# Kernel optimization log

Measured on AMD Instinct MI355X. Metric: run time of the kernel, lower is better.

The kernel has to match this reference:

```python
import jax, jax.numpy as jnp
import numpy as np

QMAX = 127.0   # 8-bit symmetric quantization
BN_EPS = 1e-5
MID = 576      # in_channels * 6 expansion


def act_fake_quant(x):
    """Per-tensor symmetric 8-bit fake-quant of activations (HAWQ QuantAct).
    Returns dequantized value and the scaling factor. STE for gradients."""
    s = jax.lax.stop_gradient(jnp.max(jnp.abs(x)) / QMAX + 1e-8)
    q = jnp.clip(jnp.round(x / s), -QMAX, QMAX) * s
    return x + jax.lax.stop_gradient(q - x), s


def fold_bn(w, gamma, beta, mean, var):
    """Fold BN into conv weights/bias (QuantBnConv2d.set_param math)."""
    f = gamma / jnp.sqrt(var + BN_EPS)
    return w * f[:, None, None, None], beta - mean * f


def weight_fake_quant(w):
    """Per-output-channel symmetric 8-bit fake-quant of folded weights."""
    s = jax.lax.stop_gradient(jnp.max(jnp.abs(w), axis=(1, 2, 3)) / QMAX + 1e-8)
    sb = s[:, None, None, None]
    q = jnp.clip(jnp.round(w / sb), -QMAX, QMAX) * sb
    return w + jax.lax.stop_gradient(q - w), s


def qbn_conv(x, w, gamma, beta, mean, var, stride, groups, pad):
    """BN-folded, weight-quantized conv (QuantBnConv2d forward)."""
    wf, bf = fold_bn(w, gamma, beta, mean, var)
    wq, ws = weight_fake_quant(wf)
    y = jax.lax.conv_general_dilated(
        x, wq, window_strides=(stride, stride), padding=pad,
        dimension_numbers=('NCHW', 'OIHW', 'NCHW'), feature_group_count=groups)
    return y + bf[None, :, None, None], ws


def setup_inputs() -> dict:
    key = jax.random.key(0)
    ks = jax.random.split(key, 16)
    C_in, C_out = 96, 96
    d = {'x': jax.random.normal(ks[0], (64, C_in, 28, 28), jnp.float32)}
    def bn(k, c):
        k1, k2, k3, k4 = jax.random.split(k, 4)
        return (1.0 + 0.1 * jax.random.normal(k1, (c,), jnp.float32),   # gamma
                0.1 * jax.random.normal(k2, (c,), jnp.float32),          # beta
                0.1 * jax.random.normal(k3, (c,), jnp.float32),          # running mean
                0.5 + jax.random.uniform(k4, (c,), jnp.float32))         # running var
    # conv1: 1x1 expansion 96 -> 576
    d['w1'] = 0.1 * jax.random.normal(ks[1], (MID, C_in, 1, 1), jnp.float32)
    d['g1'], d['b1'], d['m1'], d['v1'] = bn(ks[2], MID)
    # conv2: 3x3 depthwise, groups=576
    d['w2'] = 0.1 * jax.random.normal(ks[3], (MID, 1, 3, 3), jnp.float32)
    d['g2'], d['b2'], d['m2'], d['v2'] = bn(ks[4], MID)
    # conv3: 1x1 projection 576 -> 96
    d['w3'] = 0.1 * jax.random.normal(ks[5], (C_out, MID, 1, 1), jnp.float32)
    d['g3'], d['b3'], d['m3'], d['v3'] = bn(ks[6], C_out)
    return d


def reference(x, w1, g1, b1, m1, v1, w2, g2, b2, m2, v2, w3, g3, b3, m3, v3):
    identity = x
    # quant_act on input
    y, act_sf = act_fake_quant(x)
    # conv1 (1x1 expansion) + ReLU6 + quant_act1
    y, _ = qbn_conv(y, w1, g1, b1, m1, v1, stride=1, groups=1, pad='VALID')
    y = jnp.clip(y, 0.0, 6.0)
    y, _ = act_fake_quant(y)
    # conv2 (3x3 depthwise) + ReLU6 + quant_act2
    y, _ = qbn_conv(y, w2, g2, b2, m2, v2, stride=1, groups=MID,
                    pad=((1, 1), (1, 1)))
    y = jnp.clip(y, 0.0, 6.0)
    y, _ = act_fake_quant(y)
    # conv3 (1x1 projection, linear)
    y, _ = qbn_conv(y, w3, g3, b3, m3, v3, stride=1, groups=1, pad='VALID')
    # residual add + quant_act_int32 requantization
    y = y + identity
    y, out_sf = act_fake_quant(y)
    return y, out_sf
```

## Files before the change

### kernel.cpp

```cpp
#include <hip/hip_runtime.h>
#include <hip/hip_fp16.h>

#define CIN   96
#define MIDC  576
#define COUT  96
#define HW    784
#define W28   28
#define NX    4816896

typedef __attribute__((ext_vector_type(8))) short short8;
typedef __attribute__((ext_vector_type(4))) float floatx4;


__device__ __forceinline__ float wave_max64(float v){
  #pragma unroll
  for(int i=32;i>=1;i>>=1) v = fmaxf(v, __shfl_xor(v, i, 64));
  return v;
}

__device__ __forceinline__ void block_max_atomic(float v, unsigned* dst){
  v = wave_max64(v);
  __shared__ float sm[8];
  int lane = threadIdx.x & 63, w = threadIdx.x >> 6;
  if(lane==0) sm[w] = v;
  __syncthreads();
  if(threadIdx.x==0){
    int nw = (blockDim.x + 63) >> 6;
    float m = sm[0];
    for(int i=1;i<nw;i++) m = fmaxf(m, sm[i]);
    atomicMax(dst, __float_as_uint(m));
  }
}

__device__ __forceinline__ float fq(float x, float s){
  float q = rintf(x / s);
  q = fminf(fmaxf(q, -127.f), 127.f);
  return q * s;
}

__device__ __forceinline__ float qint(float x, float s){
  return fminf(fmaxf(rintf(x / s), -127.f), 127.f);
}

__device__ __forceinline__ float qintr(float x, float r){
  return fminf(fmaxf(rintf(x * r), -127.f), 127.f);
}

__device__ __forceinline__ ushort f2bf(float f){
  return (ushort)(__float_as_uint(f) >> 16);
}


__global__ __launch_bounds__(256) void k_prep(
    const float* __restrict__ w1,const float* __restrict__ g1,const float* __restrict__ b1,const float* __restrict__ m1,const float* __restrict__ v1,
    const float* __restrict__ w2,const float* __restrict__ g2,const float* __restrict__ b2,const float* __restrict__ m2,const float* __restrict__ v2,
    const float* __restrict__ w3,const float* __restrict__ g3,const float* __restrict__ b3,const float* __restrict__ m3,const float* __restrict__ v3,
    ushort* __restrict__ qw1, float* __restrict__ sc1, float* __restrict__ bq1,
    float*  __restrict__ wq2, float* __restrict__ bq2,
    ushort* __restrict__ qw3, float* __restrict__ sc3, float* __restrict__ bq3,
    const float4* __restrict__ xv, unsigned* umax)
{
  int b = blockIdx.x, tid = threadIdx.x;
  if(b >= 1248){
    float m = 0.f;
    for(int i = (b-1248)*256 + tid; i < NX/4; i += 512*256){
      float4 v = xv[i];
      m = fmaxf(m, fmaxf(fmaxf(fabsf(v.x), fabsf(v.y)), fmaxf(fabsf(v.z), fabsf(v.w))));
    }
    block_max_atomic(m, umax);
    return;
  }
  if(tid >= 64) return;
  int lane = tid;
  if(b < MIDC){
    int o = b;
    float f = g1[o] / sqrtf(v1[o] + 1e-5f);
    float x0 = w1[o*CIN + lane] * f;
    float x1 = (lane < 32) ? w1[o*CIN + 64 + lane] * f : 0.f;
    float m = wave_max64(fmaxf(fabsf(x0), fabsf(x1)));
    float s = m / 127.f + 1e-8f;
    qw1[o*CIN + lane] = f2bf(qint(x0, s));
    if(lane < 32) qw1[o*CIN + 64 + lane] = f2bf(qint(x1, s));
    if(lane==0){ sc1[o] = s; bq1[o] = b1[o] - m1[o]*f; }
  } else if(b < 2*MIDC){
    int c = b - MIDC;
    float f = g2[c] / sqrtf(v2[c] + 1e-5f);
    float x0 = (lane < 9) ? w2[c*9 + lane] * f : 0.f;
    float m = wave_max64(fabsf(x0));
    float s = m / 127.f + 1e-8f;
    if(lane < 9) wq2[c*9 + lane] = fq(x0, s);
    if(lane==0) bq2[c] = b2[c] - m2[c]*f;
  } else {
    int o = b - 2*MIDC;
    float f = g3[o] / sqrtf(v3[o] + 1e-5f);
    float xs[9]; float m = 0.f;
    #pragma unroll
    for(int k=0;k<9;k++){ int c = lane + 64*k; xs[k] = w3[o*MIDC + c] * f; m = fmaxf(m, fabsf(xs[k])); }
    m = wave_max64(m);
    float s = m / 127.f + 1e-8f;
    #pragma unroll
    for(int k=0;k<9;k++){ int c = lane + 64*k; qw3[o*MIDC + c] = f2bf(qint(xs[k], s)); }
    if(lane==0){ sc3[o] = s; bq3[o] = b3[o] - m3[o]*f; }
  }
}

__global__ __launch_bounds__(256) void k_quantxT(const float* __restrict__ x,
    const unsigned* __restrict__ umax, ushort* __restrict__ qxT)
{
  __shared__ ushort lds[56*100];
  int n = blockIdx.x, pc = blockIdx.y, tid = threadIdx.x;
  float s0 = __uint_as_float(umax[0])/127.f + 1e-8f;
  float r0 = 1.f/s0;
  for(int i = tid; i < 96*56; i += 256){
    int c = i/56, p = i - c*56;
    float v = x[(size_t)(n*CIN + c)*HW + pc*56 + p];
    lds[p*100 + c] = f2bf(qintr(v, r0));
  }
  __syncthreads();
  const uint* lu = (const uint*)lds;
  for(int i = tid; i < 56*12; i += 256){
    int r = i/12, cb = i - r*12;
    const uint* lr = lu + r*50 + cb*4;
    uint4 v; v.x = lr[0]; v.y = lr[1]; v.z = lr[2]; v.w = lr[3];
    *(uint4*)(qxT + ((size_t)(n*12 + cb)*HW + pc*56 + r)*8) = v;
  }
}

__global__ __launch_bounds__(256) void k_conv1(const ushort* __restrict__ qxT,
    const ushort* __restrict__ qw1, const float* __restrict__ sc1, const float* __restrict__ bq1,
    unsigned* umax, __half* __restrict__ y1T)
{
  int n = blockIdx.x, mt = blockIdx.y;
  int w = threadIdx.x >> 6, l = threadIdx.x & 63;
  int lhi = l >> 4, llo = l & 15;
  int m0 = mt*64 + w*16;
  float s0 = __uint_as_float(umax[0])/127.f + 1e-8f;
  short8 a[3];
  #pragma unroll
  for(int ks=0; ks<3; ks++)
    a[ks] = *(const short8*)(qw1 + (m0 + llo)*CIN + ks*32 + lhi*8);
  float scf[4], bf[4];
  #pragma unroll
  for(int r=0;r<4;r++){ int o = m0 + lhi*4 + r; scf[r] = s0*sc1[o]; bf[r] = bq1[o]; }
  int cgbase = (m0 >> 3) + (lhi >> 1);
  int c8base = (lhi & 1) * 4;
  float tmax = 0.f;
  for(int ch=0; ch<7; ch++){
    int p0 = ch*112;
    floatx4 acc[7];
    #pragma unroll
    for(int f=0;f<7;f++) acc[f] = (floatx4){0.f,0.f,0.f,0.f};
    #pragma unroll
    for(int ks=0; ks<3; ks++){
      #pragma unroll
      for(int f=0; f<7; f++){
        const short8 b = *(const short8*)(qxT + ((size_t)(n*12 + ks*4 + lhi)*HW + p0 + f*16 + llo)*8);
        acc[f] = __builtin_amdgcn_mfma_f32_16x16x32_bf16(a[ks], b, acc[f], 0, 0, 0);
      }
    }
    #pragma unroll
    for(int f=0; f<7; f++){
      uint pk0 = 0, pk1 = 0;
      #pragma unroll
      for(int r=0;r<4;r++){
        float v = fmaf(acc[f][r], scf[r], bf[r]);
        v = fminf(fmaxf(v, 0.f), 6.f);
        tmax = fmaxf(tmax, v);
        uint hb = (uint)__half_as_ushort(__float2half(v));
        if(r==0) pk0 = hb;        else if(r==1) pk0 |= hb<<16;
        else if(r==2) pk1 = hb;   else pk1 |= hb<<16;
      }
      uint2 pk; pk.x = pk0; pk.y = pk1;
      *(uint2*)((ushort*)y1T + ((size_t)(n*72 + cgbase)*HW + p0 + f*16 + llo)*8 + c8base) = pk;
    }
  }
  block_max_atomic(tmax, umax + 1);
}

__global__ __launch_bounds__(256) void k_conv2(const __half* __restrict__ y1T,
    const float* __restrict__ wq2, const float* __restrict__ bq2,
    unsigned* umax, __half* __restrict__ y2T)
{
  __shared__ ushort tile[2][30*30*8];
  int cg = blockIdx.x >> 4, nb = (blockIdx.x & 15) << 2;
  int tid = threadIdx.x;
  float s1 = __uint_as_float(umax[1])/127.f + 1e-8f;
  float r1 = 1.f/s1;
  const float* wc = wq2 + cg*72;
  const float* bc = bq2 + cg*8;
  float tmax = 0.f;

  #pragma unroll
  for(int bfi=0; bfi<2; bfi++){
    uint4* t4z = (uint4*)tile[bfi];
    if(tid < 116){
      int h, w;
      if(tid < 30){ h = 0; w = tid; }
      else if(tid < 60){ h = 29; w = tid - 30; }
      else if(tid < 88){ h = tid - 59; w = 0; }
      else { h = tid - 87; w = 29; }
      t4z[h*30 + w] = (uint4){0u,0u,0u,0u};
    }
  }

  uint4 ld[4];
  {
    const uint4* g4 = (const uint4*)(y1T + (size_t)(nb*72 + cg)*HW*8);
    #pragma unroll
    for(int i=0;i<4;i++){ int p = tid + i*256; if(p < HW) ld[i] = g4[p]; }
    uint4* t4 = (uint4*)tile[0];
    #pragma unroll
    for(int i=0;i<4;i++){
      int p = tid + i*256;
      if(p < HW){
        int h = p/W28, w = p - h*W28;
        uint rw[4] = {ld[i].x, ld[i].y, ld[i].z, ld[i].w};
        uint pk[4];
        #pragma unroll
        for(int j=0;j<4;j++){
          float lo = __half2float(__ushort_as_half((ushort)(rw[j] & 0xffffu)));
          float hi = __half2float(__ushort_as_half((ushort)(rw[j] >> 16)));
          uint qlo = (uint)__half_as_ushort(__float2half(rintf(lo * r1)));
          uint qhi = (uint)__half_as_ushort(__float2half(rintf(hi * r1)));
          pk[j] = (qhi << 16) | qlo;
        }
        t4[(h+1)*30 + (w+1)] = (uint4){pk[0], pk[1], pk[2], pk[3]};
      }
    }
  }

  int cur = 0;
  for(int it=0; it<4; it++){
    int n = nb + it;
    if(it < 3){
      const uint4* g4 = (const uint4*)(y1T + (size_t)((n+1)*72 + cg)*HW*8);
      #pragma unroll
      for(int i=0;i<4;i++){ int p = tid + i*256; if(p < HW) ld[i] = g4[p]; }
    }
    __syncthreads();
    const uint4* t4 = (const uint4*)tile[cur];
    uint4* o4 = (uint4*)(y2T + (size_t)(n*72 + cg)*HW*8);
    #pragma unroll
    for(int i=0;i<4;i++){
      int p = tid + i*256;
      if(p < HW){
        int h = p/W28, w = p - h*W28;
        float acc[8];
        #pragma unroll
        for(int c=0;c<8;c++) acc[c] = 0.f;
        #pragma unroll
        for(int dy=0; dy<3; dy++){
          #pragma unroll
          for(int dx=0; dx<3; dx++){
            uint4 v = t4[(h+dy)*30 + (w+dx)];
            uint rw[4] = {v.x, v.y, v.z, v.w};
            #pragma unroll
            for(int j=0;j<4;j++){
              float lo = __half2float(__ushort_as_half((ushort)(rw[j] & 0xffffu)));
              float hi = __half2float(__ushort_as_half((ushort)(rw[j] >> 16)));
              acc[2*j]   = fmaf(lo, wc[(2*j)*9   + dy*3 + dx], acc[2*j]);
              acc[2*j+1] = fmaf(hi, wc[(2*j+1)*9 + dy*3 + dx], acc[2*j+1]);
            }
          }
        }
        uint pk[4];
        #pragma unroll
        for(int j=0;j<4;j++){
          float o0 = fmaf(acc[2*j],   s1, bc[2*j]);
          float o1 = fmaf(acc[2*j+1], s1, bc[2*j+1]);
          o0 = fminf(fmaxf(o0, 0.f), 6.f);
          o1 = fminf(fmaxf(o1, 0.f), 6.f);
          tmax = fmaxf(tmax, fmaxf(o0, o1));
          uint lo = (uint)__half_as_ushort(__float2half(o0));
          uint hi = (uint)__half_as_ushort(__float2half(o1));
          pk[j] = (hi << 16) | lo;
        }
        o4[p] = (uint4){pk[0], pk[1], pk[2], pk[3]};
      }
    }
    if(it < 3){
      uint4* t4n = (uint4*)tile[cur ^ 1];
      #pragma unroll
      for(int i=0;i<4;i++){
        int p = tid + i*256;
        if(p < HW){
          int h = p/W28, w = p - h*W28;
          uint rw[4] = {ld[i].x, ld[i].y, ld[i].z, ld[i].w};
          uint pk[4];
          #pragma unroll
          for(int j=0;j<4;j++){
            float lo = __half2float(__ushort_as_half((ushort)(rw[j] & 0xffffu)));
            float hi = __half2float(__ushort_as_half((ushort)(rw[j] >> 16)));
            uint qlo = (uint)__half_as_ushort(__float2half(rintf(lo * r1)));
            uint qhi = (uint)__half_as_ushort(__float2half(rintf(hi * r1)));
            pk[j] = (qhi << 16) | qlo;
          }
          t4n[(h+1)*30 + (w+1)] = (uint4){pk[0], pk[1], pk[2], pk[3]};
        }
      }
    }
    cur ^= 1;
  }
  block_max_atomic(tmax, umax + 2);
}

__global__ __launch_bounds__(384) void k_conv3(const __half* __restrict__ y2T,
    const ushort* __restrict__ qw3, const float* __restrict__ sc3, const float* __restrict__ bq3,
    const float* __restrict__ x, unsigned* umax, float* __restrict__ out)
{
  __shared__ ushort lds[24*64*8];
  int n = blockIdx.x, pc = blockIdx.y, tid = threadIdx.x;
  int w = tid >> 6, l = tid & 63;
  int lhi = l >> 4, llo = l & 15;
  int m0 = w*16;
  int p0 = pc*56;
  float s2 = __uint_as_float(umax[2])/127.f + 1e-8f;
  float r2 = 1.f/s2;
  uint4* l4 = (uint4*)lds;
  if(tid < 192){
    int cl = tid >> 3, px = 56 + (tid & 7);
    l4[cl*64 + px] = (uint4){0u,0u,0u,0u};
  }
  float scf[4], bf[4];
  #pragma unroll
  for(int r=0;r<4;r++){ int o = m0 + lhi*4 + r; scf[r] = s2*sc3[o]; bf[r] = bq3[o]; }
  floatx4 acc[4];
  #pragma unroll
  for(int f=0;f<4;f++) acc[f] = (floatx4){0.f,0.f,0.f,0.f};

  uint4 ld[4];
  #pragma unroll
  for(int i=0;i<4;i++){
    int idx = tid + i*384;
    if(idx < 24*56){
      int cl = idx/56, r = idx - cl*56;
      ld[i] = *(const uint4*)((const ushort*)y2T + ((size_t)(n*72 + cl)*HW + p0 + r)*8);
    }
  }
  for(int ck=0; ck<3; ck++){
    if(ck > 0) __syncthreads();
    #pragma unroll
    for(int i=0;i<4;i++){
      int idx = tid + i*384;
      if(idx < 24*56){
        int cl = idx/56, r = idx - cl*56;
        uint rw[4] = {ld[i].x, ld[i].y, ld[i].z, ld[i].w};
        uint pk[4];
        #pragma unroll
        for(int j=0;j<4;j++){
          float lo = __half2float(__ushort_as_half((ushort)(rw[j] & 0xffffu)));
          float hi = __half2float(__ushort_as_half((ushort)(rw[j] >> 16)));
          uint qlo = (uint)f2bf(rintf(lo * r2));
          uint qhi = (uint)f2bf(rintf(hi * r2));
          pk[j] = (qhi << 16) | qlo;
        }
        l4[cl*64 + r] = (uint4){pk[0], pk[1], pk[2], pk[3]};
      }
    }
    if(ck < 2){
      #pragma unroll
      for(int i=0;i<4;i++){
        int idx = tid + i*384;
        if(idx < 24*56){
          int cl = idx/56, r = idx - cl*56;
          ld[i] = *(const uint4*)((const ushort*)y2T + ((size_t)(n*72 + (ck+1)*24 + cl)*HW + p0 + r)*8);
        }
      }
    }
    __syncthreads();
    #pragma unroll
    for(int ks=0; ks<6; ks++){
      const short8 a = *(const short8*)(qw3 + (m0 + llo)*MIDC + ck*192 + ks*32 + lhi*8);
      #pragma unroll
      for(int f=0; f<4; f++){
        const short8 b = *(const short8*)(lds + ((ks*4 + lhi)*64 + f*16 + llo)*8);
        acc[f] = __builtin_amdgcn_mfma_f32_16x16x32_bf16(a, b, acc[f], 0, 0, 0);
      }
    }
  }
  float tmax = 0.f;
  #pragma unroll
  for(int f=0; f<4; f++){
    if(f*16 + llo < 56){
      #pragma unroll
      for(int r=0;r<4;r++){
        size_t idx = (size_t)(n*COUT + m0 + lhi*4 + r)*HW + p0 + f*16 + llo;
        float v = fmaf(acc[f][r], scf[r], bf[r]) + x[idx];
        tmax = fmaxf(tmax, fabsf(v));
        out[idx] = v;
      }
    }
  }
  block_max_atomic(tmax, umax + 3);
}

__global__ void k_finalq(float* __restrict__ out, const unsigned* __restrict__ umax, float* __restrict__ sf){
  int i = blockIdx.x*256 + threadIdx.x;
  float s3 = __uint_as_float(umax[3]) / 127.f + 1e-8f;
  float4* o4 = (float4*)out;
  float4 v = o4[i];
  v.x = fq(v.x, s3); v.y = fq(v.y, s3); v.z = fq(v.z, s3); v.w = fq(v.w, s3);
  o4[i] = v;
  if(i == 0) *sf = s3;
}


extern "C" void kernel_launch(void* const* d_in, const int* in_sizes, int n_in,
                              void* d_out, int out_size, void* d_ws, size_t ws_size,
                              hipStream_t stream)
{
  const float* x  = (const float*)d_in[0];
  const float* w1 = (const float*)d_in[1];
  const float* g1 = (const float*)d_in[2];
  const float* b1 = (const float*)d_in[3];
  const float* m1 = (const float*)d_in[4];
  const float* v1 = (const float*)d_in[5];
  const float* w2 = (const float*)d_in[6];
  const float* g2 = (const float*)d_in[7];
  const float* b2 = (const float*)d_in[8];
  const float* m2 = (const float*)d_in[9];
  const float* v2 = (const float*)d_in[10];
  const float* w3 = (const float*)d_in[11];
  const float* g3 = (const float*)d_in[12];
  const float* b3 = (const float*)d_in[13];
  const float* m3 = (const float*)d_in[14];
  const float* v3 = (const float*)d_in[15];

  char* ws = (char*)d_ws;
  unsigned* umax = (unsigned*)(ws + 0);
  float* sc1  = (float*)(ws + 256);
  float* bq1  = (float*)(ws + 2560);
  float* bq2  = (float*)(ws + 4864);
  float* wq2  = (float*)(ws + 7168);
  float* sc3  = (float*)(ws + 27904);
  float* bq3  = (float*)(ws + 28288);
  ushort* qw1 = (ushort*)(ws + 28672);
  ushort* qw3 = (ushort*)(ws + 139264);
  ushort* qxT = (ushort*)(ws + 249856);
  __half* y1T  = (__half*)(ws + 9883648);
  __half* y2T  = (__half*)(ws + 67686400);

  float* outp = (float*)d_out;

  hipMemsetAsync(umax, 0, 16, stream);
  k_prep<<<1760, 256, 0, stream>>>(w1,g1,b1,m1,v1, w2,g2,b2,m2,v2, w3,g3,b3,m3,v3,
                                   qw1,sc1,bq1, wq2,bq2, qw3,sc3,bq3,
                                   (const float4*)x, umax);
  k_quantxT<<<dim3(64,14), 256, 0, stream>>>(x, umax, qxT);
  k_conv1<<<dim3(64,9), 256, 0, stream>>>(qxT, qw1, sc1, bq1, umax, y1T);
  k_conv2<<<1152, 256, 0, stream>>>(y1T, wq2, bq2, umax, y2T);
  k_conv3<<<dim3(64,14), 384, 0, stream>>>(y2T, qw3, sc3, bq3, x, umax, outp);
  k_finalq<<<NX/4/256, 256, 0, stream>>>(outp, umax, outp + NX);
}
```

Measured before the change: 136.1 us.

## Fuse input quantization and transpose into conv1 via LDS tile

Removes the separate input quantize/transpose kernel and its bf16 intermediate buffer. Each conv1 block now loads a 56-pixel slice of fp32 input, quantizes it into LDS in the MFMA-friendly layout, and loops over all 576 output channels from LDS. This saves one launch and a global write and read of the quantized input. In exchange the 1x1 weights are reloaded per block, and the 16-wide MFMA tiles pad 56 pixels up to 64, wasting some MFMA work.

```diff
diff --git a/kernel.cpp b/kernel.cpp
--- a/kernel.cpp
+++ b/kernel.cpp
@@ -104,74 +104,72 @@
   }
 }
 
-__global__ __launch_bounds__(256) void k_quantxT(const float* __restrict__ x,
-    const unsigned* __restrict__ umax, ushort* __restrict__ qxT)
-{
-  __shared__ ushort lds[56*100];
-  int n = blockIdx.x, pc = blockIdx.y, tid = threadIdx.x;
-  float s0 = __uint_as_float(umax[0])/127.f + 1e-8f;
-  float r0 = 1.f/s0;
-  for(int i = tid; i < 96*56; i += 256){
-    int c = i/56, p = i - c*56;
-    float v = x[(size_t)(n*CIN + c)*HW + pc*56 + p];
-    lds[p*100 + c] = f2bf(qintr(v, r0));
-  }
-  __syncthreads();
-  const uint* lu = (const uint*)lds;
-  for(int i = tid; i < 56*12; i += 256){
-    int r = i/12, cb = i - r*12;
-    const uint* lr = lu + r*50 + cb*4;
-    uint4 v; v.x = lr[0]; v.y = lr[1]; v.z = lr[2]; v.w = lr[3];
-    *(uint4*)(qxT + ((size_t)(n*12 + cb)*HW + pc*56 + r)*8) = v;
-  }
-}
-
-__global__ __launch_bounds__(256) void k_conv1(const ushort* __restrict__ qxT,
+__global__ __launch_bounds__(384) void k_conv1f(const float* __restrict__ x,
     const ushort* __restrict__ qw1, const float* __restrict__ sc1, const float* __restrict__ bq1,
     unsigned* umax, __half* __restrict__ y1T)
 {
-  int n = blockIdx.x, mt = blockIdx.y;
-  int w = threadIdx.x >> 6, l = threadIdx.x & 63;
+  __shared__ ushort bt[12*64*8];
+  int n = blockIdx.x, pc = blockIdx.y, tid = threadIdx.x;
+  int w = tid >> 6, l = tid & 63;
   int lhi = l >> 4, llo = l & 15;
-  int m0 = mt*64 + w*16;
+  int p0 = pc*56;
   float s0 = __uint_as_float(umax[0])/127.f + 1e-8f;
-  short8 a[3];
-  #pragma unroll
-  for(int ks=0; ks<3; ks++)
-    a[ks] = *(const short8*)(qw1 + (m0 + llo)*CIN + ks*32 + lhi*8);
-  float scf[4], bf[4];
-  #pragma unroll
-  for(int r=0;r<4;r++){ int o = m0 + lhi*4 + r; scf[r] = s0*sc1[o]; bf[r] = bq1[o]; }
-  int cgbase = (m0 >> 3) + (lhi >> 1);
-  int c8base = (lhi & 1) * 4;
+  float r0 = 1.f/s0;
+  if(tid < 96){
+    int cb = tid >> 3, px = 56 + (tid & 7);
+    uint4 z; z.x=0u; z.y=0u; z.z=0u; z.w=0u;
+    *(uint4*)(bt + (cb*64 + px)*8) = z;
+  }
+  for(int i = tid; i < 96*14; i += 384){
+    int c = i/14, q = i - c*14;
+    float4 v = *(const float4*)(x + (size_t)(n*CIN + c)*HW + p0 + q*4);
+    int cb = c >> 3, c8 = c & 7;
+    ushort* bp = bt + (cb*64 + q*4)*8 + c8;
+    bp[0]  = f2bf(qintr(v.x, r0));
+    bp[8]  = f2bf(qintr(v.y, r0));
+    bp[16] = f2bf(qintr(v.z, r0));
+    bp[24] = f2bf(qintr(v.w, r0));
+  }
+  __syncthreads();
   float tmax = 0.f;
-  for(int ch=0; ch<7; ch++){
-    int p0 = ch*112;
-    floatx4 acc[7];
-    #pragma unroll
-    for(int f=0;f<7;f++) acc[f] = (floatx4){0.f,0.f,0.f,0.f};
+  for(int mt=0; mt<6; mt++){
+    int m0 = mt*96 + w*16;
+    short8 a[3];
+    #pragma unroll
+    for(int ks=0; ks<3; ks++)
+      a[ks] = *(const short8*)(qw1 + (m0 + llo)*CIN + ks*32 + lhi*8);
+    float scf[4], bf[4];
+    #pragma unroll
+    for(int r=0;r<4;r++){ int o = m0 + lhi*4 + r; scf[r] = s0*sc1[o]; bf[r] = bq1[o]; }
+    floatx4 acc[4];
+    #pragma unroll
+    for(int f=0;f<4;f++) acc[f] = (floatx4){0.f,0.f,0.f,0.f};
     #pragma unroll
     for(int ks=0; ks<3; ks++){
       #pragma unroll
-      for(int f=0; f<7; f++){
-        const short8 b = *(const short8*)(qxT + ((size_t)(n*12 + ks*4 + lhi)*HW + p0 + f*16 + llo)*8);
+      for(int f=0; f<4; f++){
+        const short8 b = *(const short8*)(bt + ((ks*4 + lhi)*64 + f*16 + llo)*8);
         acc[f] = __builtin_amdgcn_mfma_f32_16x16x32_bf16(a[ks], b, acc[f], 0, 0, 0);
       }
     }
-    #pragma unroll
-    for(int f=0; f<7; f++){
-      uint pk0 = 0, pk1 = 0;
-      #pragma unroll
-      for(int r=0;r<4;r++){
-        float v = fmaf(acc[f][r], scf[r], bf[r]);
-        v = fminf(fmaxf(v, 0.f), 6.f);
-        tmax = fmaxf(tmax, v);
-        uint hb = (uint)__half_as_ushort(__float2half(v));
-        if(r==0) pk0 = hb;        else if(r==1) pk0 |= hb<<16;
-        else if(r==2) pk1 = hb;   else pk1 |= hb<<16;
-      }
-      uint2 pk; pk.x = pk0; pk.y = pk1;
-      *(uint2*)((ushort*)y1T + ((size_t)(n*72 + cgbase)*HW + p0 + f*16 + llo)*8 + c8base) = pk;
+    int cgbase = (m0 >> 3) + (lhi >> 1);
+    int c8base = (lhi & 1) * 4;
+    #pragma unroll
+    for(int f=0; f<4; f++){
+      if(f*16 + llo < 56){
+        uint pk0 = 0, pk1 = 0;
+        #pragma unroll
+        for(int r=0;r<4;r++){
+          float v = fmaf(acc[f][r], scf[r], bf[r]);
+          v = fminf(fmaxf(v, 0.f), 6.f);
+          tmax = fmaxf(tmax, v);
+          uint hb = (uint)__half_as_ushort(__float2half(v));
+          if(r==0) pk0 = hb;        else if(r==1) pk0 |= hb<<16;
+          else if(r==2) pk1 = hb;   else pk1 |= hb<<16;
+        }
+        uint2 pk; pk.x = pk0; pk.y = pk1;
+        *(uint2*)((ushort*)y1T + ((size_t)(n*72 + cgbase)*HW + p0 + f*16 + llo)*8 + c8base) = pk;
+      }
     }
   }
   block_max_atomic(tmax, umax + 1);
@@ -436,9 +434,8 @@
   float* bq3  = (float*)(ws + 28288);
   ushort* qw1 = (ushort*)(ws + 28672);
   ushort* qw3 = (ushort*)(ws + 139264);
-  ushort* qxT = (ushort*)(ws + 249856);
-  __half* y1T  = (__half*)(ws + 9883648);
-  __half* y2T  = (__half*)(ws + 67686400);
+  __half* y1T = (__half*)(ws + 9883648);
+  __half* y2T = (__half*)(ws + 67686400);
 
   float* outp = (float*)d_out;
 
@@ -446,8 +443,7 @@
   k_prep<<<1760, 256, 0, stream>>>(w1,g1,b1,m1,v1, w2,g2,b2,m2,v2, w3,g3,b3,m3,v3,
                                    qw1,sc1,bq1, wq2,bq2, qw3,sc3,bq3,
                                    (const float4*)x, umax);
-  k_quantxT<<<dim3(64,14), 256, 0, stream>>>(x, umax, qxT);
-  k_conv1<<<dim3(64,9), 256, 0, stream>>>(qxT, qw1, sc1, bq1, umax, y1T);
+  k_conv1f<<<dim3(64,14), 384, 0, stream>>>(x, qw1, sc1, bq1, umax, y1T);
   k_conv2<<<1152, 256, 0, stream>>>(y1T, wq2, bq2, umax, y2T);
   k_conv3<<<dim3(64,14), 384, 0, stream>>>(y2T, qw3, sc3, bq3, x, umax, outp);
   k_finalq<<<NX/4/256, 256, 0, stream>>>(outp, umax, outp + NX);
```

Result: faster. 117.9 us (-13.4%).
